# Performance work log

Measured on AMD Instinct MI355X. Metric: run time of the kernel, lower is better.

## Reference

```python
import jax, jax.numpy as jnp
import numpy as np

DIM = 1024
NUM_HEADS = 16
HEAD_DIM = DIM // NUM_HEADS  # 64
H = 32
W = 32
NREG = 8
B = 8
N = H * W + NREG  # 1032


def setup_inputs() -> dict:
    key = jax.random.key(0)
    ks = jax.random.split(key, 6)
    def rn(k, shape, std):
        return jax.random.normal(k, shape, dtype=jnp.float32) * std
    return {
        "x": rn(ks[0], (B, N, DIM), 1.0),
        "qkv_w": rn(ks[1], (3 * DIM, DIM), 0.02),
        "qkv_b": jnp.zeros((3 * DIM,), jnp.float32),
        "proj_w": rn(ks[2], (DIM, DIM), 0.02),
        "proj_b": jnp.zeros((DIM,), jnp.float32),
        "rel_pos_h": rn(ks[3], (2 * H - 1, HEAD_DIM), 0.02),
        "rel_pos_w": rn(ks[4], (2 * W - 1, HEAD_DIM), 0.02),
        "nreg": NREG,
        "cait": 0,
    }


def _rel_pos_table(rel_pos, size):
    # q_size == k_size == size -> relative index = i - j + (size - 1)
    coords = jnp.arange(size)[:, None] - jnp.arange(size)[None, :] + (size - 1)
    return rel_pos[coords]  # (size, size, head_dim)


def reference(x, qkv_w, qkv_b, proj_w, proj_b, rel_pos_h, rel_pos_w, nreg, cait):
    Bx, Nx, C = x.shape
    hd = C // NUM_HEADS
    scale = hd ** (-0.5)
    # qkv: (B, N, 3, nH, hd) -> (3, nH, B, N, hd) -> (3, nH*B, N, hd)
    qkv = (x @ qkv_w.T + qkv_b).reshape(Bx, Nx, 3, NUM_HEADS, hd)
    qkv = jnp.transpose(qkv, (2, 3, 0, 1, 4)).reshape(3, NUM_HEADS * Bx, Nx, hd)
    q, k, v = qkv[0], qkv[1], qkv[2]
    if cait:
        q = q[:, -nreg:]
    attn = jnp.einsum('bqd,bkd->bqk', q * scale, k)  # (nH*B, Nq, N)
    if not cait:
        hw = H * W
        Rh = _rel_pos_table(rel_pos_h, H)  # (H, H, hd)
        Rw = _rel_pos_table(rel_pos_w, W)  # (W, W, hd)
        r_q = q[:, :hw].reshape(-1, H, W, hd)  # unscaled q, grid tokens only
        rel_h = jnp.einsum('bhwc,hkc->bhwk', r_q, Rh)
        rel_w = jnp.einsum('bhwc,wkc->bhwk', r_q, Rw)
        grid = (attn[:, :hw, :hw].reshape(-1, H, W, H, W)
                + rel_h[:, :, :, :, None] + rel_w[:, :, :, None, :])
        attn = attn.at[:, :hw, :hw].set(grid.reshape(-1, hw, hw))
    attn = jax.nn.softmax(attn, axis=-1)
    out = jnp.einsum('bqk,bkd->bqd', attn, v)  # (nH*B, Nq, hd)
    out = out.reshape(NUM_HEADS, Bx, -1, hd)
    out = jnp.transpose(out, (1, 2, 0, 3)).reshape(Bx, -1, C)
    return out @ proj_w.T + proj_b
```

## Files before the change

kernel.cpp:

```cpp
#include <hip/hip_runtime.h>

#define BATCH 8
#define NTOK 1032
#define NPAD 1152
#define MTOT (BATCH*NTOK)
#define MPAD 8320

#define SCALE_Q 0.18033688011112042f
#define C2      5.770780163555854f

typedef __bf16 bf16x8 __attribute__((ext_vector_type(8)));
typedef float f32x4 __attribute__((ext_vector_type(4)));
typedef unsigned short us8 __attribute__((ext_vector_type(8)));
typedef unsigned short us4 __attribute__((ext_vector_type(4)));
typedef short s4 __attribute__((ext_vector_type(4)));

__device__ __forceinline__ unsigned short f2bf(float f){
  unsigned int u = __builtin_bit_cast(unsigned int, f);
  u += 0x7fffu + ((u >> 16) & 1u);
  return (unsigned short)(u >> 16);
}
__device__ __forceinline__ float bf2f(unsigned short u){
  return __builtin_bit_cast(float, (unsigned int)u << 16);
}

#define MFMA16(a,b,c) __builtin_amdgcn_mfma_f32_16x16x32_bf16( \
    __builtin_bit_cast(bf16x8,(a)), __builtin_bit_cast(bf16x8,(b)), (c), 0, 0, 0)
#define MFMAH(a,b,c) __builtin_amdgcn_mfma_f32_16x16x16bf16_1k( \
    __builtin_bit_cast(s4,(a)), __builtin_bit_cast(s4,(b)), (c), 0, 0, 0)

__device__ __forceinline__ void gl_lds16(const unsigned short* g, unsigned short* l){
  __builtin_amdgcn_global_load_lds(
      (const __attribute__((address_space(1))) unsigned int*)g,
      (__attribute__((address_space(3))) unsigned int*)l, 16, 0, 0);
}

__global__ __launch_bounds__(256) void cvt_f32_bf16(const float* __restrict__ in,
                                                    unsigned short* __restrict__ out, int n4){
  int i = blockIdx.x * 256 + threadIdx.x;
  if (i < n4){
    float4 v = reinterpret_cast<const float4*>(in)[i];
    us4 o; o.x = f2bf(v.x); o.y = f2bf(v.y); o.z = f2bf(v.z); o.w = f2bf(v.w);
    reinterpret_cast<us4*>(out)[i] = o;
  }
}

__global__ __launch_bounds__(256) void pad_zero(unsigned short* __restrict__ qb,
                                                unsigned short* __restrict__ kb,
                                                unsigned short* __restrict__ xb,
                                                unsigned short* __restrict__ ao){
  int i = blockIdx.x * 256 + threadIdx.x;
  const int t1 = 128 * (NPAD - NTOK) * 64;
  const int t2 = t1 + (MPAD - MTOT) * 1024;
  const int t3 = t2 + (MPAD - MTOT) * 1024;
  if (i < t1){
    int bh = i / ((NPAD - NTOK) * 64);
    int r  = (i / 64) % (NPAD - NTOK);
    int d  = i % 64;
    int idx = (bh * NPAD + NTOK + r) * 64 + d;
    qb[idx] = 0;
    kb[idx] = 0;
  } else if (i < t2){
    xb[(size_t)MTOT * 1024 + (i - t1)] = 0;
  } else if (i < t3){
    ao[(size_t)MTOT * 1024 + (i - t2)] = 0;
  }
}

__global__ __launch_bounds__(256,3) void qkv_gemm(
    const unsigned short* __restrict__ A,
    const unsigned short* __restrict__ Bw,
    const float* __restrict__ bias,
    unsigned short* __restrict__ qb,
    unsigned short* __restrict__ kb,
    unsigned short* __restrict__ vb)
{
  const int K = 1024;
  __shared__ __align__(16) unsigned short As[2][128*32];
  __shared__ __align__(16) unsigned short Bs[2][128*32];
  int tid = threadIdx.x;
  int id = blockIdx.x;
  int work = (id & 7) * 195 + (id >> 3);
  int m0 = (work / 24) * 128, n0 = (work % 24) * 128;
  int w = tid >> 6, lane = tid & 63, lr = lane & 15, lg = lane >> 4;
  int wr = w >> 1, wc = w & 1;
  int srow = lane >> 2, scol = (lane & 3) * 8;
  f32x4 acc[4][4] = {};

  #pragma unroll
  for (int i = 0; i < 2; i++){
    int q = w * 2 + i;
    gl_lds16(&A [(size_t)(m0 + q*16 + srow) * K + scol], &As[0][q*512]);
    gl_lds16(&Bw[(size_t)(n0 + q*16 + srow) * K + scol], &Bs[0][q*512]);
  }
  __syncthreads();

  for (int kt = 0; kt < 32; kt++){
    int cur = kt & 1;
    if (kt < 31){
      int k0 = (kt + 1) * 32;
      #pragma unroll
      for (int i = 0; i < 2; i++){
        int q = w * 2 + i;
        gl_lds16(&A [(size_t)(m0 + q*16 + srow) * K + k0 + scol], &As[cur^1][q*512]);
        gl_lds16(&Bw[(size_t)(n0 + q*16 + srow) * K + k0 + scol], &Bs[cur^1][q*512]);
      }
    }
    us8 a[4], b[4];
    #pragma unroll
    for (int mi = 0; mi < 4; mi++) a[mi] = *reinterpret_cast<const us8*>(&As[cur][(wr*64 + mi*16 + lr)*32 + lg*8]);
    #pragma unroll
    for (int ni = 0; ni < 4; ni++) b[ni] = *reinterpret_cast<const us8*>(&Bs[cur][(wc*64 + ni*16 + lr)*32 + lg*8]);
    #pragma unroll
    for (int mi = 0; mi < 4; mi++)
      #pragma unroll
      for (int ni = 0; ni < 4; ni++)
        acc[mi][ni] = MFMA16(a[mi], b[ni], acc[mi][ni]);
    __syncthreads();
  }

  #pragma unroll
  for (int mi = 0; mi < 4; mi++){
    #pragma unroll
    for (int ni = 0; ni < 4; ni++){
      #pragma unroll
      for (int reg = 0; reg < 4; reg++){
        int m = m0 + wr*64 + mi*16 + lg*4 + reg;
        if (m >= MTOT) continue;
        int n = n0 + wc*64 + ni*16 + lr;
        float val = acc[mi][ni][reg] + bias[n];
        int b_ = m / NTOK, nidx = m % NTOK;
        int t = n >> 10, h = (n >> 6) & 15, d = n & 63;
        int bh = h * BATCH + b_;
        if (t == 0){
          qb[(size_t)(bh * NPAD + nidx) * 64 + d] = f2bf(val * SCALE_Q);
        } else if (t == 1){
          kb[(size_t)(bh * NPAD + nidx) * 64 + d] = f2bf(val);
        } else {
          vb[(size_t)(bh * NTOK + nidx) * 64 + d] = f2bf(val);
        }
      }
    }
  }
}

__global__ __launch_bounds__(256) void transpose_v(const unsigned short* __restrict__ vb,
                                                   unsigned short* __restrict__ vt){
  __shared__ unsigned short Ls[64][72];
  int blk = blockIdx.x;
  int bh = blk / 17, tl = blk % 17;
  int n0 = tl * 64;
  int t = threadIdx.x;

  #pragma unroll
  for (int p = 0; p < 2; p++){
    int idx = p * 256 + t;
    int r = idx >> 3, c = idx & 7;
    us8 v = {};
    if (n0 + r < NTOK)
      v = *reinterpret_cast<const us8*>(&vb[((size_t)bh * NTOK + n0 + r) * 64 + c * 8]);
    *reinterpret_cast<us8*>(&Ls[r][c * 8]) = v;
  }
  __syncthreads();

  int d = t & 63, ng = t >> 6;
  us8 o[2];
  #pragma unroll
  for (int hf = 0; hf < 2; hf++){
    #pragma unroll
    for (int j = 0; j < 8; j++) o[hf][j] = Ls[ng*16 + hf*8 + j][d];
    *reinterpret_cast<us8*>(&vt[((size_t)bh * 64 + d) * NPAD + n0 + ng*16 + hf*8]) = o[hf];
  }
}

__global__ __launch_bounds__(256,3) void attn_kernel(
    const unsigned short* __restrict__ qb,
    const unsigned short* __restrict__ kb,
    const unsigned short* __restrict__ vt,
    const float* __restrict__ rph,
    const float* __restrict__ rpw,
    unsigned short* __restrict__ ao)
{
  __shared__ __align__(16) unsigned short Ks[2][64*64];
  __shared__ __align__(16) unsigned short Vs[2][64*64];
  __shared__ unsigned short RHt[32*128];
  __shared__ unsigned short RWc[32*128];

  int id = blockIdx.x;
  int work = (id & 7) * 144 + (id >> 3);
  int bh = work / 9;
  int qt = work % 9;
  int tid = threadIdx.x, w = tid >> 6, lane = tid & 63, lr = lane & 15, lg = lane >> 4;
  int h = bh >> 3, b_ = bh & 7;

  const unsigned short* qbase = qb + (size_t)bh * NPAD * 64;
  const unsigned short* kbase = kb + (size_t)bh * NPAD * 64;
  const unsigned short* vbase = vt + (size_t)bh * 64 * NPAD;

  #pragma unroll
  for (int t = 0; t < 2; t++){
    int i = t*256 + tid;
    int row = i >> 3, cs = (i & 7) ^ (row & 7);
    gl_lds16(&kbase[(size_t)row*64 + cs*8],   &Ks[0][(t*256 + w*64)*8]);
    gl_lds16(&vbase[(size_t)row*NPAD + cs*8], &Vs[0][(t*256 + w*64)*8]);
  }

  us8 aq[2][2];
  #pragma unroll
  for (int qf = 0; qf < 2; qf++){
    int qrow = qt*128 + w*32 + qf*16 + lr;
    aq[qf][0] = *reinterpret_cast<const us8*>(&qbase[(size_t)qrow*64 + lg*8]);
    aq[qf][1] = *reinterpret_cast<const us8*>(&qbase[(size_t)qrow*64 + 32 + lg*8]);
  }

  float rwreg[2][2][4] = {};

  if (qt < 8){
    int qh = qt*4 + w;
    f32x4 accH[2][2] = {};
    #pragma unroll
    for (int ks = 0; ks < 2; ks++){
      #pragma unroll
      for (int nf2 = 0; nf2 < 2; nf2++){
        int t = nf2*16 + lr;
        const float* src = rph + (size_t)(qh - t + 31)*64 + ks*32 + lg*8;
        us8 ar;
        #pragma unroll
        for (int j = 0; j < 8; j++) ar[j] = f2bf(src[j]);
        #pragma unroll
        for (int qf = 0; qf < 2; qf++) accH[qf][nf2] = MFMA16(ar, aq[qf][ks], accH[qf][nf2]);
      }
    }
    #pragma unroll
    for (int qf = 0; qf < 2; qf++)
      #pragma unroll
      for (int nf2 = 0; nf2 < 2; nf2++)
        #pragma unroll
        for (int reg = 0; reg < 4; reg++){
          int t_out = nf2*16 + lg*4 + reg;
          RHt[t_out*128 + w*32 + qf*16 + lr] = f2bf(accH[qf][nf2][reg] * 8.0f);
        }
    f32x4 accW[2][4] = {};
    #pragma unroll
    for (int ks = 0; ks < 2; ks++){
      #pragma unroll
      for (int nf = 0; nf < 4; nf++){
        int t = nf*16 + lr;
        us8 aw_ = {};
        if (t < 63){
          const float* src = rpw + (size_t)t*64 + ks*32 + lg*8;
          #pragma unroll
          for (int j = 0; j < 8; j++) aw_[j] = f2bf(src[j]);
        }
        #pragma unroll
        for (int qf = 0; qf < 2; qf++) accW[qf][nf] = MFMA16(aw_, aq[qf][ks], accW[qf][nf]);
      }
    }
    #pragma unroll
    for (int qf = 0; qf < 2; qf++)
      #pragma unroll
      for (int nf = 0; nf < 4; nf++)
        #pragma unroll
        for (int reg = 0; reg < 4; reg++){
          int t_out = nf*16 + lg*4 + reg;
          int qw = qf*16 + lr;
          int kw = qw - t_out + 31;
          if (kw >= 0 && kw < 32)
            RWc[kw*128 + w*32 + qf*16 + lr] = f2bf(accW[qf][nf][reg] * 8.0f);
        }
    #pragma unroll
    for (int qf = 0; qf < 2; qf++)
      #pragma unroll
      for (int hf = 0; hf < 2; hf++)
        #pragma unroll
        for (int reg = 0; reg < 4; reg++)
          rwreg[qf][hf][reg] = bf2f(RWc[(hf*16 + lg*4 + reg)*128 + w*32 + qf*16 + lr]);
  }
  __syncthreads();

  f32x4 O[2][4] = {};
  f32x4 lac[2] = {};
  s4 ones4;
  ones4.x = (short)0x3F80; ones4.y = (short)0x3F80; ones4.z = (short)0x3F80; ones4.w = (short)0x3F80;

  for (int kt = 0; kt < 17; kt++){
    int cur = kt & 1;
    if (kt < 16){
      #pragma unroll
      for (int t = 0; t < 2; t++){
        int i = t*256 + tid;
        int row = i >> 3, cs = (i & 7) ^ (row & 7);
        gl_lds16(&kbase[(size_t)((kt+1)*64 + row)*64 + cs*8], &Ks[cur^1][(t*256 + w*64)*8]);
        gl_lds16(&vbase[(size_t)row*NPAD + (kt+1)*64 + cs*8], &Vs[cur^1][(t*256 + w*64)*8]);
      }
    }

    f32x4 S[2][4] = {};
    __builtin_amdgcn_s_setprio(1);
    #pragma unroll
    for (int ks = 0; ks < 2; ks++)
      #pragma unroll
      for (int nf = 0; nf < 4; nf++){
        us8 bk = *reinterpret_cast<const us8*>(
            &Ks[cur][(nf*16 + lr)*64 + (((ks*4 + lg) ^ (lr & 7)) * 8)]);
        S[0][nf] = MFMA16(bk, aq[0][ks], S[0][nf]);
        S[1][nf] = MFMA16(bk, aq[1][ks], S[1][nf]);
      }
    __builtin_amdgcn_s_setprio(0);

    bool gk = (qt < 8) && (kt < 16);
    float rh2[2][2];
    #pragma unroll
    for (int qf = 0; qf < 2; qf++)
      #pragma unroll
      for (int hf = 0; hf < 2; hf++)
        rh2[qf][hf] = gk ? (bf2f(RHt[(kt*2 + hf)*128 + w*32 + qf*16 + lr]) - C2) : -C2;

    s4 pa[2][4];
    #pragma unroll
    for (int qf = 0; qf < 2; qf++){
      #pragma unroll
      for (int nf = 0; nf < 4; nf++){
        float pv[4];
        #pragma unroll
        for (int reg = 0; reg < 4; reg++){
          float logit = S[qf][nf][reg] + rh2[qf][nf>>1] + (gk ? rwreg[qf][nf&1][reg] : 0.f);
          float p = __builtin_amdgcn_exp2f(logit);
          int key = kt*64 + nf*16 + lg*4 + reg;
          pv[reg] = (key < NTOK) ? p : 0.f;
        }
        unsigned int u0 = __builtin_amdgcn_perm(
            __builtin_bit_cast(unsigned int, pv[1]), __builtin_bit_cast(unsigned int, pv[0]), 0x07060302u);
        unsigned int u1 = __builtin_amdgcn_perm(
            __builtin_bit_cast(unsigned int, pv[3]), __builtin_bit_cast(unsigned int, pv[2]), 0x07060302u);
        uint2 uu; uu.x = u0; uu.y = u1;
        pa[qf][nf] = __builtin_bit_cast(s4, uu);
      }
    }

    __builtin_amdgcn_s_setprio(1);
    #pragma unroll
    for (int qf = 0; qf < 2; qf++)
      #pragma unroll
      for (int nf = 0; nf < 4; nf++)
        lac[qf] = MFMAH(pa[qf][nf], ones4, lac[qf]);
    #pragma unroll
    for (int nf = 0; nf < 4; nf++){
      #pragma unroll
      for (int nfd = 0; nfd < 4; nfd++){
        us4 bv = *reinterpret_cast<const us4*>(
            &Vs[cur][(nfd*16 + lr)*64 + (((nf*2 + (lg>>1)) ^ (lr & 7))*8) + (lg&1)*4]);
        O[0][nfd] = MFMAH(pa[0][nf], bv, O[0][nfd]);
        O[1][nfd] = MFMAH(pa[1][nf], bv, O[1][nfd]);
      }
    }
    __builtin_amdgcn_s_setprio(0);
    __syncthreads();
  }

  #pragma unroll
  for (int qf = 0; qf < 2; qf++)
    #pragma unroll
    for (int reg = 0; reg < 4; reg++){
      int qg = qt*128 + w*32 + qf*16 + lg*4 + reg;
      if (qg < NTOK){
        float inv = 1.0f / lac[qf][reg];
        #pragma unroll
        for (int nfd = 0; nfd < 4; nfd++)
          ao[(size_t)(b_ * NTOK + qg) * 1024 + h*64 + nfd*16 + lr] = f2bf(O[qf][nfd][reg] * inv);
      }
    }
}

__global__ __launch_bounds__(256,3) void proj_gemm(
    const unsigned short* __restrict__ A,
    const unsigned short* __restrict__ Bw,
    const float* __restrict__ bias,
    float* __restrict__ out)
{
  const int K = 1024;
  __shared__ __align__(16) unsigned short As[2][128*32];
  __shared__ __align__(16) unsigned short Bs[2][128*32];
  int tid = threadIdx.x;
  int id = blockIdx.x;
  int work = (id & 7) * 65 + (id >> 3);
  int m0 = (work / 8) * 128, n0 = (work % 8) * 128;
  int w = tid >> 6, lane = tid & 63, lr = lane & 15, lg = lane >> 4;
  int wr = w >> 1, wc = w & 1;
  int srow = lane >> 2, scol = (lane & 3) * 8;
  f32x4 acc[4][4] = {};

  #pragma unroll
  for (int i = 0; i < 2; i++){
    int q = w * 2 + i;
    gl_lds16(&A [(size_t)(m0 + q*16 + srow) * K + scol], &As[0][q*512]);
    gl_lds16(&Bw[(size_t)(n0 + q*16 + srow) * K + scol], &Bs[0][q*512]);
  }
  __syncthreads();

  for (int kt = 0; kt < 32; kt++){
    int cur = kt & 1;
    if (kt < 31){
      int k0 = (kt + 1) * 32;
      #pragma unroll
      for (int i = 0; i < 2; i++){
        int q = w * 2 + i;
        gl_lds16(&A [(size_t)(m0 + q*16 + srow) * K + k0 + scol], &As[cur^1][q*512]);
        gl_lds16(&Bw[(size_t)(n0 + q*16 + srow) * K + k0 + scol], &Bs[cur^1][q*512]);
      }
    }
    us8 a[4], b[4];
    #pragma unroll
    for (int mi = 0; mi < 4; mi++) a[mi] = *reinterpret_cast<const us8*>(&As[cur][(wr*64 + mi*16 + lr)*32 + lg*8]);
    #pragma unroll
    for (int ni = 0; ni < 4; ni++) b[ni] = *reinterpret_cast<const us8*>(&Bs[cur][(wc*64 + ni*16 + lr)*32 + lg*8]);
    #pragma unroll
    for (int mi = 0; mi < 4; mi++)
      #pragma unroll
      for (int ni = 0; ni < 4; ni++)
        acc[mi][ni] = MFMA16(a[mi], b[ni], acc[mi][ni]);
    __syncthreads();
  }

  #pragma unroll
  for (int mi = 0; mi < 4; mi++){
    #pragma unroll
    for (int ni = 0; ni < 4; ni++){
      #pragma unroll
      for (int reg = 0; reg < 4; reg++){
        int m = m0 + wr*64 + mi*16 + lg*4 + reg;
        if (m >= MTOT) continue;
        int n = n0 + wc*64 + ni*16 + lr;
        out[(size_t)m * 1024 + n] = acc[mi][ni][reg] + bias[n];
      }
    }
  }
}

extern "C" void kernel_launch(void* const* d_in, const int* in_sizes, int n_in,
                              void* d_out, int out_size, void* d_ws, size_t ws_size,
                              hipStream_t stream)
{
  const float* x      = (const float*)d_in[0];
  const float* qkv_w  = (const float*)d_in[1];
  const float* qkv_b  = (const float*)d_in[2];
  const float* proj_w = (const float*)d_in[3];
  const float* proj_b = (const float*)d_in[4];
  const float* rph    = (const float*)d_in[5];
  const float* rpw    = (const float*)d_in[6];
  float* out = (float*)d_out;

  char* ws = (char*)d_ws;
  size_t off = 0;
  auto alloc = [&](size_t bytes){ char* p = ws + off; off += (bytes + 255) & ~(size_t)255; return p; };
  unsigned short* x_bf  = (unsigned short*)alloc((size_t)MPAD * 1024 * 2);
  unsigned short* qw_bf = (unsigned short*)alloc((size_t)3072 * 1024 * 2);
  unsigned short* pw_bf = (unsigned short*)alloc((size_t)1024 * 1024 * 2);
  unsigned short* qbuf  = (unsigned short*)alloc((size_t)128 * NPAD * 64 * 2);
  unsigned short* kbuf  = (unsigned short*)alloc((size_t)128 * NPAD * 64 * 2);
  unsigned short* vtbuf = (unsigned short*)alloc((size_t)128 * 64 * NPAD * 2);
  unsigned short* aout  = (unsigned short*)alloc((size_t)MPAD * 1024 * 2);
  if (off > ws_size) return;

  unsigned short* vbuf = aout;

  int n4x = MTOT * 1024 / 4;
  cvt_f32_bf16<<<dim3((n4x + 255) / 256), 256, 0, stream>>>(x, x_bf, n4x);
  int n4q = 3072 * 1024 / 4;
  cvt_f32_bf16<<<dim3((n4q + 255) / 256), 256, 0, stream>>>(qkv_w, qw_bf, n4q);
  int n4p = 1024 * 1024 / 4;
  cvt_f32_bf16<<<dim3((n4p + 255) / 256), 256, 0, stream>>>(proj_w, pw_bf, n4p);

  int npad = 128 * (NPAD - NTOK) * 64 + 2 * (MPAD - MTOT) * 1024;
  pad_zero<<<dim3((npad + 255) / 256), 256, 0, stream>>>(qbuf, kbuf, x_bf, aout);

  qkv_gemm<<<dim3(1560), 256, 0, stream>>>(x_bf, qw_bf, qkv_b, qbuf, kbuf, vbuf);
  transpose_v<<<dim3(128 * 17), 256, 0, stream>>>(vbuf, vtbuf);
  attn_kernel<<<dim3(1152), 256, 0, stream>>>(qbuf, kbuf, vtbuf, rph, rpw, aout);
  proj_gemm<<<dim3(520), 256, 0, stream>>>(aout, pw_bf, proj_b, out);
}
```

Measured before the change: 230.9 us.

## Use partial vmcnt waits, swizzle GEMM LDS tiles, raise occupancy bound

The GEMM and attention loops now wait only on the older batch of global-to-LDS loads (vmcnt(4)) before the barrier, so the next tile's prefetch stays in flight during compute instead of being drained by __syncthreads. The GEMM LDS tiles get an XOR swizzle on the 16-byte column chunk, applied the same way on store and load, to reduce bank conflicts. The GEMM launch bounds go from 3 to 4 blocks per SM. The risks are register pressure at the higher occupancy and correctness of the hand-written waitcnt and barrier ordering.

```diff
diff --git a/kernel.cpp b/kernel.cpp
--- a/kernel.cpp
+++ b/kernel.cpp
@@ -67,7 +67,7 @@
   }
 }
 
-__global__ __launch_bounds__(256,3) void qkv_gemm(
+__global__ __launch_bounds__(256,4) void qkv_gemm(
     const unsigned short* __restrict__ A,
     const unsigned short* __restrict__ Bw,
     const float* __restrict__ bias,
@@ -84,7 +84,9 @@
   int m0 = (work / 24) * 128, n0 = (work % 24) * 128;
   int w = tid >> 6, lane = tid & 63, lr = lane & 15, lg = lane >> 4;
   int wr = w >> 1, wc = w & 1;
-  int srow = lane >> 2, scol = (lane & 3) * 8;
+  int srow = lane >> 2;
+  int scol = ((lane & 3) ^ ((lane >> 3) & 3)) * 8;
+  int sa = (lg ^ ((lr >> 1) & 3)) * 8;
   f32x4 acc[4][4] = {};
 
   #pragma unroll
@@ -93,7 +95,6 @@
     gl_lds16(&A [(size_t)(m0 + q*16 + srow) * K + scol], &As[0][q*512]);
     gl_lds16(&Bw[(size_t)(n0 + q*16 + srow) * K + scol], &Bs[0][q*512]);
   }
-  __syncthreads();
 
   for (int kt = 0; kt < 32; kt++){
     int cur = kt & 1;
@@ -105,18 +106,24 @@
         gl_lds16(&A [(size_t)(m0 + q*16 + srow) * K + k0 + scol], &As[cur^1][q*512]);
         gl_lds16(&Bw[(size_t)(n0 + q*16 + srow) * K + k0 + scol], &Bs[cur^1][q*512]);
       }
-    }
+      asm volatile("s_waitcnt vmcnt(4)" ::: "memory");
+    } else {
+      asm volatile("s_waitcnt vmcnt(0)" ::: "memory");
+    }
+    __builtin_amdgcn_sched_barrier(0);
+    __builtin_amdgcn_s_barrier();
+
     us8 a[4], b[4];
     #pragma unroll
-    for (int mi = 0; mi < 4; mi++) a[mi] = *reinterpret_cast<const us8*>(&As[cur][(wr*64 + mi*16 + lr)*32 + lg*8]);
-    #pragma unroll
-    for (int ni = 0; ni < 4; ni++) b[ni] = *reinterpret_cast<const us8*>(&Bs[cur][(wc*64 + ni*16 + lr)*32 + lg*8]);
+    for (int mi = 0; mi < 4; mi++) a[mi] = *reinterpret_cast<const us8*>(&As[cur][(wr*64 + mi*16 + lr)*32 + sa]);
+    #pragma unroll
+    for (int ni = 0; ni < 4; ni++) b[ni] = *reinterpret_cast<const us8*>(&Bs[cur][(wc*64 + ni*16 + lr)*32 + sa]);
     #pragma unroll
     for (int mi = 0; mi < 4; mi++)
       #pragma unroll
       for (int ni = 0; ni < 4; ni++)
         acc[mi][ni] = MFMA16(a[mi], b[ni], acc[mi][ni]);
-    __syncthreads();
+    __builtin_amdgcn_s_barrier();
   }
 
   #pragma unroll
@@ -293,7 +300,12 @@
         gl_lds16(&kbase[(size_t)((kt+1)*64 + row)*64 + cs*8], &Ks[cur^1][(t*256 + w*64)*8]);
         gl_lds16(&vbase[(size_t)row*NPAD + (kt+1)*64 + cs*8], &Vs[cur^1][(t*256 + w*64)*8]);
       }
-    }
+      asm volatile("s_waitcnt vmcnt(4)" ::: "memory");
+    } else {
+      asm volatile("s_waitcnt vmcnt(0)" ::: "memory");
+    }
+    __builtin_amdgcn_sched_barrier(0);
+    __builtin_amdgcn_s_barrier();
 
     f32x4 S[2][4] = {};
     __builtin_amdgcn_s_setprio(1);
@@ -355,7 +367,7 @@
       }
     }
     __builtin_amdgcn_s_setprio(0);
-    __syncthreads();
+    __builtin_amdgcn_s_barrier();
   }
 
   #pragma unroll
@@ -372,7 +384,7 @@
     }
 }
 
-__global__ __launch_bounds__(256,3) void proj_gemm(
+__global__ __launch_bounds__(256,4) void proj_gemm(
     const unsigned short* __restrict__ A,
     const unsigned short* __restrict__ Bw,
     const float* __restrict__ bias,
@@ -387,7 +399,9 @@
   int m0 = (work / 8) * 128, n0 = (work % 8) * 128;
   int w = tid >> 6, lane = tid & 63, lr = lane & 15, lg = lane >> 4;
   int wr = w >> 1, wc = w & 1;
-  int srow = lane >> 2, scol = (lane & 3) * 8;
+  int srow = lane >> 2;
+  int scol = ((lane & 3) ^ ((lane >> 3) & 3)) * 8;
+  int sa = (lg ^ ((lr >> 1) & 3)) * 8;
   f32x4 acc[4][4] = {};
 
   #pragma unroll
@@ -396,7 +410,6 @@
     gl_lds16(&A [(size_t)(m0 + q*16 + srow) * K + scol], &As[0][q*512]);
     gl_lds16(&Bw[(size_t)(n0 + q*16 + srow) * K + scol], &Bs[0][q*512]);
   }
-  __syncthreads();
 
   for (int kt = 0; kt < 32; kt++){
     int cur = kt & 1;
@@ -408,18 +421,24 @@
         gl_lds16(&A [(size_t)(m0 + q*16 + srow) * K + k0 + scol], &As[cur^1][q*512]);
         gl_lds16(&Bw[(size_t)(n0 + q*16 + srow) * K + k0 + scol], &Bs[cur^1][q*512]);
       }
-    }
+      asm volatile("s_waitcnt vmcnt(4)" ::: "memory");
+    } else {
+      asm volatile("s_waitcnt vmcnt(0)" ::: "memory");
+    }
+    __builtin_amdgcn_sched_barrier(0);
+    __builtin_amdgcn_s_barrier();
+
     us8 a[4], b[4];
     #pragma unroll
-    for (int mi = 0; mi < 4; mi++) a[mi] = *reinterpret_cast<const us8*>(&As[cur][(wr*64 + mi*16 + lr)*32 + lg*8]);
-    #pragma unroll
-    for (int ni = 0; ni < 4; ni++) b[ni] = *reinterpret_cast<const us8*>(&Bs[cur][(wc*64 + ni*16 + lr)*32 + lg*8]);
+    for (int mi = 0; mi < 4; mi++) a[mi] = *reinterpret_cast<const us8*>(&As[cur][(wr*64 + mi*16 + lr)*32 + sa]);
+    #pragma unroll
+    for (int ni = 0; ni < 4; ni++) b[ni] = *reinterpret_cast<const us8*>(&Bs[cur][(wc*64 + ni*16 + lr)*32 + sa]);
     #pragma unroll
     for (int mi = 0; mi < 4; mi++)
       #pragma unroll
       for (int ni = 0; ni < 4; ni++)
         acc[mi][ni] = MFMA16(a[mi], b[ni], acc[mi][ni]);
-    __syncthreads();
+    __builtin_amdgcn_s_barrier();
   }
 
   #pragma unroll
```

Measured after the change: 226.0 us. 1.02x faster.
